# Kernel optimization log

Measured on AMD Instinct MI355X. Metric: run time of the kernel, lower is better.

## Reference

```python
import jax, jax.numpy as jnp
import numpy as np

B, S, H = 32, 512, 256
NUM_BINS = 256
MAX_LEN = 4096  # static pad length = S * max_duration (8); original pads to data-dependent max

def _quantize(values, num_bins, v_min, v_max):
    # torch.bucketize(right=False) == searchsorted side='left' on linspace boundaries
    v = jnp.clip(values, v_min, v_max)
    boundaries = jnp.linspace(v_min, v_max, num_bins)
    bins = jnp.searchsorted(boundaries, v, side='left')
    return jnp.clip(bins, 0, num_bins - 1)

def _length_regulate(x, duration_target):
    # x: [B,S,H]; durations rounded, clamped >=1
    dur = jnp.maximum(jnp.round(duration_target).astype(jnp.int32), 1)  # [B,S]
    cum = jnp.cumsum(dur, axis=1)                                       # [B,S]
    t = jnp.arange(MAX_LEN)                                             # [T]
    # frame t belongs to token j where cum[j-1] <= t < cum[j]
    idx = jax.vmap(lambda c: jnp.searchsorted(c, t, side='right'))(cum)  # [B,T]
    valid = (t[None, :] < cum[:, -1:]).astype(x.dtype)                   # [B,T]
    idx = jnp.clip(idx, 0, S - 1)
    out = jnp.take_along_axis(x, idx[..., None], axis=1)                 # [B,T,H]
    return out * valid[..., None]

def setup_inputs() -> dict:
    key = jax.random.key(0)
    k = jax.random.split(key, 6)
    return {
        'encoder_output': jax.random.normal(k[0], (B, S, H), jnp.float32),
        'pitch_target': 50.0 + 350.0 * jax.random.uniform(k[1], (B, S), jnp.float32),
        'energy_target': jax.random.uniform(k[2], (B, S), jnp.float32),
        'duration_target': 1.0 + 7.0 * jax.random.uniform(k[3], (B, S), jnp.float32),
        'pitch_table': 0.02 * jax.random.normal(k[4], (NUM_BINS, H), jnp.float32),
        'energy_table': 0.02 * jax.random.normal(k[5], (NUM_BINS, H), jnp.float32),
    }

def reference(encoder_output, pitch_target, energy_target, duration_target,
              pitch_table, energy_table):
    # dropout is identity in eval mode
    pitch_bins = _quantize(pitch_target, NUM_BINS, 50.0, 400.0)
    energy_bins = _quantize(energy_target, NUM_BINS, 0.0, 1.0)
    out = encoder_output + pitch_table[pitch_bins] + energy_table[energy_bins]
    return _length_regulate(out, duration_target)
```

## Files before the change

kernel.cpp:

```cpp
#include <hip/hip_runtime.h>

#define BB 32
#define SS 512
#define HH 256
#define NBINS 256
#define TMAX 4096
#define ROWS_PER_WAVE 16

__device__ __forceinline__ double boundary(int i, double vmin, double vmax, double step) {
    if (i == NBINS - 1) return vmax;
    return (double)i * step + vmin;
}

__device__ __forceinline__ int quantize_bin(float v, float vminf, float vmaxf) {
    v = fminf(fmaxf(v, vminf), vmaxf);
    double vd = (double)v;
    double vmin = (double)vminf, vmax = (double)vmaxf;
    double step = (vmax - vmin) / (double)(NBINS - 1);
    int g = (int)ceil((vd - vmin) / step);
    g = max(0, min(NBINS - 1, g));
    while (g > 0 && vd <= boundary(g - 1, vmin, vmax, step)) g--;
    while (g < NBINS - 1 && vd > boundary(g, vmin, vmax, step)) g++;
    return g;
}

__global__ __launch_bounds__(512)
void prep_kernel(const float* __restrict__ pitch,
                 const float* __restrict__ energy,
                 const float* __restrict__ dur,
                 int* __restrict__ map) {
    int b = blockIdx.x;
    int s = threadIdx.x;
    __shared__ int cum[SS];
    __shared__ int pb_sh[SS];
    __shared__ int eb_sh[SS];

    int tok = b * SS + s;
    pb_sh[s] = quantize_bin(pitch[tok], 50.0f, 400.0f);
    eb_sh[s] = quantize_bin(energy[tok], 0.0f, 1.0f);
    int d = (int)rintf(dur[tok]);
    if (d < 1) d = 1;
    cum[s] = d;
    __syncthreads();

    for (int off = 1; off < SS; off <<= 1) {
        int add = (s >= off) ? cum[s - off] : 0;
        __syncthreads();
        cum[s] += add;
        __syncthreads();
    }
    int total = cum[SS - 1];

    for (int t = s; t < TMAX; t += SS) {
        int packed;
        if (t >= total) {
            packed = -1;
        } else {
            int lo = 0, hi = SS;
            while (lo < hi) {
                int m = (lo + hi) >> 1;
                if (cum[m] <= t) lo = m + 1; else hi = m;
            }
            int j = (lo > SS - 1) ? (SS - 1) : lo;
            packed = j | (pb_sh[j] << 9) | (eb_sh[j] << 17);
        }
        map[b * TMAX + t] = packed;
    }
}

__global__ __launch_bounds__(256)
void gather_kernel(const float* __restrict__ enc,
                   const float* __restrict__ ptab,
                   const float* __restrict__ etab,
                   const int* __restrict__ map,
                   float* __restrict__ out) {
    int wave = blockIdx.x * 4 + (threadIdx.x >> 6);
    int lane = threadIdx.x & 63;
    int row0 = wave * ROWS_PER_WAVE;
    int b = row0 >> 12;

    int my_packed = (lane < ROWS_PER_WAVE) ? map[row0 + lane] : 0;

    int last_packed = -2;
    float4 val = make_float4(0.f, 0.f, 0.f, 0.f);
    float4* outv = reinterpret_cast<float4*>(out + (size_t)row0 * HH) + lane;

    #pragma unroll
    for (int r = 0; r < ROWS_PER_WAVE; ++r) {
        int packed = __shfl(my_packed, r);
        if (packed != last_packed) {
            if (packed < 0) {
                val = make_float4(0.f, 0.f, 0.f, 0.f);
            } else {
                int j  = packed & 511;
                int pb = (packed >> 9) & 255;
                int eb = (packed >> 17) & 255;
                int tok = b * SS + j;
                const float4 e = reinterpret_cast<const float4*>(enc  + (size_t)tok * HH)[lane];
                const float4 p = reinterpret_cast<const float4*>(ptab + (size_t)pb  * HH)[lane];
                const float4 q = reinterpret_cast<const float4*>(etab + (size_t)eb  * HH)[lane];
                val.x = (e.x + p.x) + q.x;
                val.y = (e.y + p.y) + q.y;
                val.z = (e.z + p.z) + q.z;
                val.w = (e.w + p.w) + q.w;
            }
            last_packed = packed;
        }
        outv[(size_t)r * (HH / 4)] = val;
    }
}

extern "C" void kernel_launch(void* const* d_in, const int* in_sizes, int n_in,
                              void* d_out, int out_size, void* d_ws, size_t ws_size,
                              hipStream_t stream) {
    const float* enc    = (const float*)d_in[0];
    const float* pitch  = (const float*)d_in[1];
    const float* energy = (const float*)d_in[2];
    const float* dur    = (const float*)d_in[3];
    const float* ptab   = (const float*)d_in[4];
    const float* etab   = (const float*)d_in[5];
    float* out = (float*)d_out;

    int* map = (int*)d_ws;

    prep_kernel<<<BB, SS, 0, stream>>>(pitch, energy, dur, map);

    int waves = (BB * TMAX) / ROWS_PER_WAVE;
    gather_kernel<<<waves / 4, 256, 0, stream>>>(enc, ptab, etab, map, out);
}
```

Baseline: 173.9 us.

## Fuse prep and gather kernels into one kernel with shared-memory row map

Merges the quantize/scan/search prep kernel into the gather kernel. Each of 512 blocks redoes the per-batch quantization and prefix scan for its batch, then computes a 256-row segment of the frame-to-token map into shared memory, and its 8 waves write 32 rows each. This removes one kernel launch, the global map round-trip and the serial 32-block prep phase, at the cost of 16x redundant quantization (double-precision math) and scanning per batch.

```diff
diff --git a/kernel.cpp b/kernel.cpp
--- a/kernel.cpp
+++ b/kernel.cpp
@@ -5,7 +5,8 @@
 #define HH 256
 #define NBINS 256
 #define TMAX 4096
-#define ROWS_PER_WAVE 16
+#define ROWS_PER_BLOCK 256
+#define RPW 32
 
 __device__ __forceinline__ double boundary(int i, double vmin, double vmax, double step) {
     if (i == NBINS - 1) return vmax;
@@ -25,15 +26,23 @@
 }
 
 __global__ __launch_bounds__(512)
-void prep_kernel(const float* __restrict__ pitch,
-                 const float* __restrict__ energy,
-                 const float* __restrict__ dur,
-                 int* __restrict__ map) {
-    int b = blockIdx.x;
-    int s = threadIdx.x;
+void fused_kernel(const float* __restrict__ enc,
+                  const float* __restrict__ pitch,
+                  const float* __restrict__ energy,
+                  const float* __restrict__ dur,
+                  const float* __restrict__ ptab,
+                  const float* __restrict__ etab,
+                  float* __restrict__ out) {
     __shared__ int cum[SS];
     __shared__ int pb_sh[SS];
     __shared__ int eb_sh[SS];
+    __shared__ int pk_sh[ROWS_PER_BLOCK];
+
+    int blk  = blockIdx.x;
+    int b    = blk >> 4;
+    int seg  = blk & 15;
+    int row0b = seg * ROWS_PER_BLOCK;
+    int s = threadIdx.x;
 
     int tok = b * SS + s;
     pb_sh[s] = quantize_bin(pitch[tok], 50.0f, 400.0f);
@@ -51,7 +60,8 @@
     }
     int total = cum[SS - 1];
 
-    for (int t = s; t < TMAX; t += SS) {
+    if (s < ROWS_PER_BLOCK) {
+        int t = row0b + s;
         int packed;
         if (t >= total) {
             packed = -1;
@@ -64,29 +74,23 @@
             int j = (lo > SS - 1) ? (SS - 1) : lo;
             packed = j | (pb_sh[j] << 9) | (eb_sh[j] << 17);
         }
-        map[b * TMAX + t] = packed;
+        pk_sh[s] = packed;
     }
-}
+    __syncthreads();
 
-__global__ __launch_bounds__(256)
-void gather_kernel(const float* __restrict__ enc,
-                   const float* __restrict__ ptab,
-                   const float* __restrict__ etab,
-                   const int* __restrict__ map,
-                   float* __restrict__ out) {
-    int wave = blockIdx.x * 4 + (threadIdx.x >> 6);
-    int lane = threadIdx.x & 63;
-    int row0 = wave * ROWS_PER_WAVE;
-    int b = row0 >> 12;
+    int wid  = s >> 6;
+    int lane = s & 63;
+    int rbase = wid * RPW;
 
-    int my_packed = (lane < ROWS_PER_WAVE) ? map[row0 + lane] : 0;
+    int my_packed = (lane < RPW) ? pk_sh[rbase + lane] : 0;
 
+    size_t grow0 = (size_t)b * TMAX + row0b + rbase;
     int last_packed = -2;
     float4 val = make_float4(0.f, 0.f, 0.f, 0.f);
-    float4* outv = reinterpret_cast<float4*>(out + (size_t)row0 * HH) + lane;
+    float4* outv = reinterpret_cast<float4*>(out + grow0 * HH) + lane;
 
     #pragma unroll
-    for (int r = 0; r < ROWS_PER_WAVE; ++r) {
+    for (int r = 0; r < RPW; ++r) {
         int packed = __shfl(my_packed, r);
         if (packed != last_packed) {
             if (packed < 0) {
@@ -95,10 +99,10 @@
                 int j  = packed & 511;
                 int pb = (packed >> 9) & 255;
                 int eb = (packed >> 17) & 255;
-                int tok = b * SS + j;
-                const float4 e = reinterpret_cast<const float4*>(enc  + (size_t)tok * HH)[lane];
-                const float4 p = reinterpret_cast<const float4*>(ptab + (size_t)pb  * HH)[lane];
-                const float4 q = reinterpret_cast<const float4*>(etab + (size_t)eb  * HH)[lane];
+                int tk = b * SS + j;
+                const float4 e = reinterpret_cast<const float4*>(enc  + (size_t)tk * HH)[lane];
+                const float4 p = reinterpret_cast<const float4*>(ptab + (size_t)pb * HH)[lane];
+                const float4 q = reinterpret_cast<const float4*>(etab + (size_t)eb * HH)[lane];
                 val.x = (e.x + p.x) + q.x;
                 val.y = (e.y + p.y) + q.y;
                 val.z = (e.z + p.z) + q.z;
@@ -121,10 +125,6 @@
     const float* etab   = (const float*)d_in[5];
     float* out = (float*)d_out;
 
-    int* map = (int*)d_ws;
-
-    prep_kernel<<<BB, SS, 0, stream>>>(pitch, energy, dur, map);
-
-    int waves = (BB * TMAX) / ROWS_PER_WAVE;
-    gather_kernel<<<waves / 4, 256, 0, stream>>>(enc, ptab, etab, map, out);
+    int blocks = (BB * TMAX) / ROWS_PER_BLOCK;
+    fused_kernel<<<blocks, 512, 0, stream>>>(enc, pitch, energy, dur, ptab, etab, out);
 }
```

Measured after the change: 170.6 us. Within noise of the previous version (-1.9%).
